# Kernel tuning notes

Hardware: AMD Instinct MI355X
Metric: run time of the kernel (lower is better)

The kernel has to match this reference:

```python
import jax, jax.numpy as jnp
import numpy as np

B, CIN, COUT, H, W, K, SDIM = 16, 256, 256, 64, 64, 3, 128

def setup_inputs() -> dict:
    key = jax.random.key(0)
    ks = jax.random.split(key, 5)
    return {
        "x": jax.random.normal(ks[0], (B, CIN, H, W), dtype=jnp.float32),
        "c_src": jax.random.normal(ks[1], (B, SDIM), dtype=jnp.float32),
        "c_trg": jax.random.normal(ks[2], (B, SDIM), dtype=jnp.float32),
        "style_w": jax.random.normal(ks[3], (CIN, SDIM), dtype=jnp.float32),
        "style_b": jnp.ones((CIN,), dtype=jnp.float32),  # bias_init=1
        "weight": jax.random.normal(ks[4], (1, COUT, CIN, K, K), dtype=jnp.float32),
    }

def reference(x, c_src, c_trg, style_w, style_b, weight):
    b, cin, h, w = x.shape
    _, cout, _, k, _ = weight.shape
    # EqualLinear: scale = 1/sqrt(dim_in)=1/sqrt(128), lr_mul=1
    lin_scale = np.float32(1.0 / np.sqrt(SDIM))
    s = c_trg @ (style_w * lin_scale).T + style_b            # [B, Cin]
    # modulate
    conv_scale = np.float32(1.0 / np.sqrt(cin * k * k))
    wmod = conv_scale * weight * s[:, None, :, None, None]   # [B, Cout, Cin, K, K]
    # demodulate
    demod = jax.lax.rsqrt(jnp.sum(wmod * wmod, axis=(2, 3, 4)) + 1e-8)  # [B, Cout]
    wmod = wmod * demod[:, :, None, None, None]
    # grouped conv with groups=batch == per-sample conv; vmap over batch
    def conv_one(xb, wb):
        # xb: [Cin,H,W], wb: [Cout,Cin,K,K]
        return jax.lax.conv_general_dilated(
            xb[None], wb, window_strides=(1, 1), padding="SAME",
            dimension_numbers=("NCHW", "OIHW", "NCHW"))[0]
    out = jax.vmap(conv_one)(x, wmod)                        # [B, Cout, H, W]
    return out
```

## Files before the change

kernel.cpp:

```cpp
#include <hip/hip_runtime.h>


#define WSH_OFF    35684352
#define S_OFF      36864000
#define G_OFF      36880384
#define DEMOD_OFF  37142528

typedef __attribute__((ext_vector_type(8))) short bf16x8;
typedef __attribute__((ext_vector_type(4))) float f32x4;
typedef __attribute__((ext_vector_type(4))) int i32x4;

#define GLOAD_LDS16(g, l)                                                        \
  __builtin_amdgcn_global_load_lds(                                              \
      (const __attribute__((address_space(1))) void*)(g),                        \
      (__attribute__((address_space(3))) void*)(l), 16, 0, 0)

__device__ __forceinline__ unsigned short f2bf(float f) {
  unsigned int u = __builtin_bit_cast(unsigned int, f);
  u += 0x7FFFu + ((u >> 16) & 1u);
  return (unsigned short)(u >> 16);
}

__global__ void prep1_k(const float* __restrict__ c_trg,
                        const float* __restrict__ style_w,
                        const float* __restrict__ style_b,
                        const float* __restrict__ weight,
                        float* __restrict__ s,
                        short* __restrict__ wsh,
                        float* __restrict__ G) {
  const int blk = blockIdx.x;
  const int tid = threadIdx.x;
  if (blk < 16) {
    const int b = blk;
    const float* ct = c_trg + b * 128;
    const float* sw = style_w + tid * 128;
    float acc = 0.f;
#pragma unroll 4
    for (int d = 0; d < 128; ++d) acc += ct[d] * sw[d];
    s[b * 256 + tid] = acc * 0.08838834764831845f + style_b[tid];
  } else {
    const int idx = (blk - 16) * 256 + tid;
    const float* wsrc = weight + idx * 9;
    float g = 0.f;
#pragma unroll
    for (int t = 0; t < 9; ++t) {
      float v = wsrc[t] * 0.020833333333333332f;
      g += v * v;
      wsh[t * 65536 + idx] = (short)f2bf(v);
    }
    G[idx] = g;
  }
}

__global__ void xpose_k(const float* __restrict__ x,
                        const float* __restrict__ s,
                        const float* __restrict__ G,
                        short* __restrict__ xpad,
                        float* __restrict__ demod) {
  __shared__ float tile[64][65];
  const int bid = blockIdx.x;
  const int tid = threadIdx.x;
  if (bid >= 4112) {
    const int id = bid - 4112;
    const int b = id >> 8, co = id & 255;
    const float sv = s[b * 256 + tid];
    float ss = G[co * 256 + tid] * sv * sv;
#pragma unroll
    for (int o = 32; o; o >>= 1) ss += __shfl_down(ss, o);
    __shared__ float red[4];
    if ((tid & 63) == 0) red[tid >> 6] = ss;
    __syncthreads();
    if (tid == 0) demod[id] = rsqrtf(red[0] + red[1] + red[2] + red[3] + 1e-8f);
    return;
  }
  if (bid >= 4096) {
    const int b = bid - 4096;
    char* base = (char*)xpad + b * 66 * 66 * 512;
    const i32x4 z = {0, 0, 0, 0};
    for (int i = tid; i < 4224; i += 256) {
      const int r = i >= 2112;
      const int off = r * (65 * 66 * 512) + (i - r * 2112) * 16;
      *(i32x4*)(base + off) = z;
    }
    for (int i = tid; i < 4096; i += 256) {
      const int h = 1 + (i >> 6);
      const int side = (i >> 5) & 1;
      const int j = i & 31;
      *(i32x4*)(base + (h * 66 + side * 65) * 512 + j * 16) = z;
    }
    return;
  }
  const int ct = bid & 3;
  const int h = (bid >> 2) & 63;
  const int b = bid >> 8;
  const int w = tid & 63, cl = tid >> 6;
  const float* src = x + ((b * 256 + ct * 64) * 64 + h) * 64;
#pragma unroll
  for (int i = 0; i < 16; ++i) {
    int c = i * 4 + cl;
    tile[c][w] = src[c * 4096 + w];
  }
  const int cp = tid & 31;
  const float s0 = s[b * 256 + ct * 64 + cp * 2];
  const float s1 = s[b * 256 + ct * 64 + cp * 2 + 1];
  __syncthreads();
  short* dst = xpad + ((b * 66 + h + 1) * 66 + 1) * 256 + ct * 64;
#pragma unroll
  for (int i = 0; i < 8; ++i) {
    int idx = i * 256 + tid;
    int w2 = idx >> 5;
    unsigned int u = (unsigned int)f2bf(tile[cp * 2][w2] * s0) |
                     ((unsigned int)f2bf(tile[cp * 2 + 1][w2] * s1) << 16);
    *(unsigned int*)(dst + w2 * 256 + cp * 2) = u;
  }
}

__global__ __launch_bounds__(512, 2) void conv_k(const short* __restrict__ xpad,
                                                 const short* __restrict__ wsh,
                                                 const float* __restrict__ demod,
                                                 float* __restrict__ out) {
  extern __shared__ __align__(16) char lds[];

  const int tid = threadIdx.x;
  const int lane = tid & 63;
  const int wid = tid >> 6;
  const int wm = wid >> 2;
  const int wn = wid & 3;

  const int orig = blockIdx.x;
  const int bid = (orig & 7) * 32 + (orig >> 3);
  const int b = bid >> 4;
  const int r0 = (bid & 15) * 4;

  const int t3 = tid >> 3;
  const int c16 = (tid & 7) * 16;
  const int swzc = c16 ^ ((t3 & 7) << 4);
  int aO[4], bO[4];
#pragma unroll
  for (int j = 0; j < 4; ++j) {
    aO[j] = (j * 64 + t3) * 512 + swzc;
    bO[j] = ((b * 66 + r0 + j) * 66 + t3) * 512 + swzc;
  }
  const char* wB = (const char*)wsh;
  const char* xB = (const char*)xpad;

  auto stageA = [&](int ts) {
    const int tap = ts >> 2, cc = ts & 3;
    const int aAdd = tap * 131072 + cc * 128;
    char* d = lds + (ts & 1) * 65536;
#pragma unroll
    for (int j = 0; j < 4; ++j)
      GLOAD_LDS16(wB + aAdd + aO[j], d + j * 8192 + tid * 16);
  };
  auto stageB = [&](int ts) {
    const int tap = ts >> 2, cc = ts & 3;
    const int dh = (tap * 11) >> 5;
    const int bAdd = (dh * 66 + (tap - dh * 3)) * 512 + cc * 128;
    char* d = lds + (ts & 1) * 65536 + 32768;
#pragma unroll
    for (int j = 0; j < 4; ++j)
      GLOAD_LDS16(xB + bAdd + bO[j], d + j * 8192 + tid * 16);
  };

  const int xall = (lane & 7) << 4;
  const int xl = xall & 0x30;
  const int xh = xall & 0x40;
  const int colR = (((lane >> 4) << 4) ^ xl);
  const int ko0 = xh;
  const int ko1 = 64 ^ xh;
  const int aRdBase = (wm * 128 + (lane & 15)) * 128 + colR;
  const int bRdBase = 32768 + (wn * 64 + (lane & 15)) * 128 + colR;

  f32x4 acc[8][4] = {};

  stageA(0);
  stageB(0);

  for (int t = 0; t < 36; ++t) {
    asm volatile("s_waitcnt vmcnt(0)" ::: "memory");
    __builtin_amdgcn_s_barrier();
    __builtin_amdgcn_sched_barrier(0);

    const char* Ab = lds + (t & 1) * 65536 + aRdBase;
    const char* Bb = lds + (t & 1) * 65536 + bRdBase;
    bf16x8 a03[4][2], a47[4][2], bq[4][2];

#pragma unroll
    for (int m = 0; m < 4; ++m) a03[m][0] = *(const bf16x8*)(Ab + m * 2048 + ko0);
#pragma unroll
    for (int n = 0; n < 4; ++n) bq[n][0] = *(const bf16x8*)(Bb + n * 2048 + ko0);
    if (t + 1 < 36) stageA(t + 1);
    __builtin_amdgcn_sched_barrier(0);

#pragma unroll
    for (int m = 0; m < 4; ++m) a03[m][1] = *(const bf16x8*)(Ab + m * 2048 + ko1);
#pragma unroll
    for (int n = 0; n < 4; ++n) bq[n][1] = *(const bf16x8*)(Bb + n * 2048 + ko1);
    if (t + 1 < 36) stageB(t + 1);
    __builtin_amdgcn_sched_barrier(0);

#pragma unroll
    for (int m = 0; m < 4; ++m)
#pragma unroll
      for (int n = 0; n < 4; ++n)
        acc[m][n] = __builtin_amdgcn_mfma_f32_16x16x32_bf16(a03[m][0], bq[n][0], acc[m][n], 0, 0, 0);
    __builtin_amdgcn_sched_barrier(0);

#pragma unroll
    for (int m = 0; m < 4; ++m) a47[m][0] = *(const bf16x8*)(Ab + (m + 4) * 2048 + ko0);
    __builtin_amdgcn_sched_barrier(0);

#pragma unroll
    for (int m = 0; m < 4; ++m)
#pragma unroll
      for (int n = 0; n < 4; ++n)
        acc[m][n] = __builtin_amdgcn_mfma_f32_16x16x32_bf16(a03[m][1], bq[n][1], acc[m][n], 0, 0, 0);
    __builtin_amdgcn_sched_barrier(0);

#pragma unroll
    for (int m = 0; m < 4; ++m) a47[m][1] = *(const bf16x8*)(Ab + (m + 4) * 2048 + ko1);
    __builtin_amdgcn_sched_barrier(0);

#pragma unroll
    for (int m = 0; m < 4; ++m)
#pragma unroll
      for (int n = 0; n < 4; ++n)
        acc[m + 4][n] = __builtin_amdgcn_mfma_f32_16x16x32_bf16(a47[m][0], bq[n][0], acc[m + 4][n], 0, 0, 0);
    __builtin_amdgcn_sched_barrier(0);

#pragma unroll
    for (int m = 0; m < 4; ++m)
#pragma unroll
      for (int n = 0; n < 4; ++n)
        acc[m + 4][n] = __builtin_amdgcn_mfma_f32_16x16x32_bf16(a47[m][1], bq[n][1], acc[m + 4][n], 0, 0, 0);
    asm volatile("" ::: "memory");
  }

  const int pc = lane & 15;
  const int rOff = (lane >> 4) * 4;
  const int h = r0 + wn;
#pragma unroll
  for (int m = 0; m < 8; ++m) {
#pragma unroll
    for (int r = 0; r < 4; ++r) {
      const int co = wm * 128 + m * 16 + rOff + r;
      const float dm = demod[(b << 8) + co];
      float* orow = out + (((b << 8) + co) << 12) + (h << 6);
#pragma unroll
      for (int n = 0; n < 4; ++n) {
        orow[n * 16 + pc] = acc[m][n][r] * dm;
      }
    }
  }
}

extern "C" void kernel_launch(void* const* d_in, const int* in_sizes, int n_in,
                              void* d_out, int out_size, void* d_ws, size_t ws_size,
                              hipStream_t stream) {
  const float* x       = (const float*)d_in[0];
  const float* c_trg   = (const float*)d_in[2];
  const float* style_w = (const float*)d_in[3];
  const float* style_b = (const float*)d_in[4];
  const float* weight  = (const float*)d_in[5];
  float* out = (float*)d_out;

  char* ws = (char*)d_ws;
  short* xpad  = (short*)(ws);
  short* wsh   = (short*)(ws + WSH_OFF);
  float* s     = (float*)(ws + S_OFF);
  float* G     = (float*)(ws + G_OFF);
  float* demod = (float*)(ws + DEMOD_OFF);

  hipFuncSetAttribute((const void*)conv_k,
                      hipFuncAttributeMaxDynamicSharedMemorySize, 131072);

  prep1_k<<<272, 256, 0, stream>>>(c_trg, style_w, style_b, weight, s, wsh, G);
  xpose_k<<<8208, 256, 0, stream>>>(x, s, G, xpad, demod);
  conv_k<<<256, 512, 131072, stream>>>(xpad, wsh, demod, out);
}
```

Before: 99.22 us.

## Load weight fragments directly from global memory instead of staging through LDS

The A operand (pre-transformed weights) is now read straight from global memory into registers for each tap and channel chunk, and the LDS double-buffering covers only the input tile. This halves LDS use and removes the LDS write/read traffic for weights, which could allow higher occupancy. It also drops the sched_barrier fences so the compiler can interleave loads and MFMAs freely. The risk is exposing global/L2 latency on the weight loads, since they are no longer prefetched one step ahead, plus less controlled instruction scheduling.

```diff
diff --git a/kernel.cpp b/kernel.cpp
--- a/kernel.cpp
+++ b/kernel.cpp
@@ -135,28 +135,18 @@
   const int t3 = tid >> 3;
   const int c16 = (tid & 7) * 16;
   const int swzc = c16 ^ ((t3 & 7) << 4);
-  int aO[4], bO[4];
-#pragma unroll
-  for (int j = 0; j < 4; ++j) {
-    aO[j] = (j * 64 + t3) * 512 + swzc;
+  int bO[4];
+#pragma unroll
+  for (int j = 0; j < 4; ++j)
     bO[j] = ((b * 66 + r0 + j) * 66 + t3) * 512 + swzc;
-  }
   const char* wB = (const char*)wsh;
   const char* xB = (const char*)xpad;
 
-  auto stageA = [&](int ts) {
-    const int tap = ts >> 2, cc = ts & 3;
-    const int aAdd = tap * 131072 + cc * 128;
-    char* d = lds + (ts & 1) * 65536;
-#pragma unroll
-    for (int j = 0; j < 4; ++j)
-      GLOAD_LDS16(wB + aAdd + aO[j], d + j * 8192 + tid * 16);
-  };
   auto stageB = [&](int ts) {
     const int tap = ts >> 2, cc = ts & 3;
     const int dh = (tap * 11) >> 5;
     const int bAdd = (dh * 66 + (tap - dh * 3)) * 512 + cc * 128;
-    char* d = lds + (ts & 1) * 65536 + 32768;
+    char* d = lds + (ts & 1) * 32768;
 #pragma unroll
     for (int j = 0; j < 4; ++j)
       GLOAD_LDS16(xB + bAdd + bO[j], d + j * 8192 + tid * 16);
@@ -168,12 +158,12 @@
   const int colR = (((lane >> 4) << 4) ^ xl);
   const int ko0 = xh;
   const int ko1 = 64 ^ xh;
-  const int aRdBase = (wm * 128 + (lane & 15)) * 128 + colR;
-  const int bRdBase = 32768 + (wn * 64 + (lane & 15)) * 128 + colR;
+  const int bRdBase = (wn * 64 + (lane & 15)) * 128 + colR;
+
+  const int aBase = (wm * 128 + (lane & 15)) * 512 + (lane >> 4) * 16;
 
   f32x4 acc[8][4] = {};
 
-  stageA(0);
   stageB(0);
 
   for (int t = 0; t < 36; ++t) {
@@ -181,58 +171,53 @@
     __builtin_amdgcn_s_barrier();
     __builtin_amdgcn_sched_barrier(0);
 
-    const char* Ab = lds + (t & 1) * 65536 + aRdBase;
-    const char* Bb = lds + (t & 1) * 65536 + bRdBase;
+    const int tap = t >> 2, cc = t & 3;
+    const char* aT = wB + tap * 131072 + cc * 128 + aBase;
+    const char* Bb = lds + (t & 1) * 32768 + bRdBase;
     bf16x8 a03[4][2], a47[4][2], bq[4][2];
 
 #pragma unroll
-    for (int m = 0; m < 4; ++m) a03[m][0] = *(const bf16x8*)(Ab + m * 2048 + ko0);
-#pragma unroll
-    for (int n = 0; n < 4; ++n) bq[n][0] = *(const bf16x8*)(Bb + n * 2048 + ko0);
-    if (t + 1 < 36) stageA(t + 1);
-    __builtin_amdgcn_sched_barrier(0);
-
-#pragma unroll
-    for (int m = 0; m < 4; ++m) a03[m][1] = *(const bf16x8*)(Ab + m * 2048 + ko1);
-#pragma unroll
-    for (int n = 0; n < 4; ++n) bq[n][1] = *(const bf16x8*)(Bb + n * 2048 + ko1);
+    for (int m = 0; m < 4; ++m) {
+      a03[m][0] = *(const bf16x8*)(aT + m * 8192);
+      a03[m][1] = *(const bf16x8*)(aT + m * 8192 + 64);
+    }
+#pragma unroll
+    for (int n = 0; n < 4; ++n) {
+      bq[n][0] = *(const bf16x8*)(Bb + n * 2048 + ko0);
+      bq[n][1] = *(const bf16x8*)(Bb + n * 2048 + ko1);
+    }
     if (t + 1 < 36) stageB(t + 1);
-    __builtin_amdgcn_sched_barrier(0);
 
 #pragma unroll
     for (int m = 0; m < 4; ++m)
 #pragma unroll
       for (int n = 0; n < 4; ++n)
         acc[m][n] = __builtin_amdgcn_mfma_f32_16x16x32_bf16(a03[m][0], bq[n][0], acc[m][n], 0, 0, 0);
-    __builtin_amdgcn_sched_barrier(0);
-
-#pragma unroll
-    for (int m = 0; m < 4; ++m) a47[m][0] = *(const bf16x8*)(Ab + (m + 4) * 2048 + ko0);
-    __builtin_amdgcn_sched_barrier(0);
+
+#pragma unroll
+    for (int m = 0; m < 4; ++m) {
+      a47[m][0] = *(const bf16x8*)(aT + (m + 4) * 8192);
+      a47[m][1] = *(const bf16x8*)(aT + (m + 4) * 8192 + 64);
+    }
 
 #pragma unroll
     for (int m = 0; m < 4; ++m)
 #pragma unroll
       for (int n = 0; n < 4; ++n)
         acc[m][n] = __builtin_amdgcn_mfma_f32_16x16x32_bf16(a03[m][1], bq[n][1], acc[m][n], 0, 0, 0);
-    __builtin_amdgcn_sched_barrier(0);
-
-#pragma unroll
-    for (int m = 0; m < 4; ++m) a47[m][1] = *(const bf16x8*)(Ab + (m + 4) * 2048 + ko1);
-    __builtin_amdgcn_sched_barrier(0);
 
 #pragma unroll
     for (int m = 0; m < 4; ++m)
 #pragma unroll
       for (int n = 0; n < 4; ++n)
         acc[m + 4][n] = __builtin_amdgcn_mfma_f32_16x16x32_bf16(a47[m][0], bq[n][0], acc[m + 4][n], 0, 0, 0);
-    __builtin_amdgcn_sched_barrier(0);
 
 #pragma unroll
     for (int m = 0; m < 4; ++m)
 #pragma unroll
       for (int n = 0; n < 4; ++n)
         acc[m + 4][n] = __builtin_amdgcn_mfma_f32_16x16x32_bf16(a47[m][1], bq[n][1], acc[m + 4][n], 0, 0, 0);
+
     asm volatile("" ::: "memory");
   }
 
@@ -272,9 +257,9 @@
   float* demod = (float*)(ws + DEMOD_OFF);
 
   hipFuncSetAttribute((const void*)conv_k,
-                      hipFuncAttributeMaxDynamicSharedMemorySize, 131072);
+                      hipFuncAttributeMaxDynamicSharedMemorySize, 65536);
 
   prep1_k<<<272, 256, 0, stream>>>(c_trg, style_w, style_b, weight, s, wsh, G);
   xpose_k<<<8208, 256, 0, stream>>>(x, s, G, xpad, demod);
-  conv_k<<<256, 512, 131072, stream>>>(xpad, wsh, demod, out);
-}
+  conv_k<<<256, 512, 65536, stream>>>(xpad, wsh, demod, out);
+}
```

Result: slower. 190.5 us (+92.0%).

## Halve conv workgroup to 4 waves with 128x128 per-wave tiles

Applied to the files above, without the earlier changes.

The conv kernel moves from 8 waves of 512 threads, each computing a 128x64 tile, to 4 waves of 256 threads, each computing a 128x128 tile with 256 accumulator registers. Staging loads double per thread to cover the same LDS tile. The interleaved sched_barrier schedule is replaced by two plain load-then-MFMA phases per K step. Each wave now reuses fragments over more MFMAs, at the cost of fewer waves to hide latency and heavy register pressure that could spill.

```diff
diff --git a/kernel.cpp b/kernel.cpp
--- a/kernel.cpp
+++ b/kernel.cpp
@@ -115,7 +115,7 @@
   }
 }
 
-__global__ __launch_bounds__(512, 2) void conv_k(const short* __restrict__ xpad,
+__global__ __launch_bounds__(256, 1) void conv_k(const short* __restrict__ xpad,
                                                  const short* __restrict__ wsh,
                                                  const float* __restrict__ demod,
                                                  float* __restrict__ out) {
@@ -124,8 +124,8 @@
   const int tid = threadIdx.x;
   const int lane = tid & 63;
   const int wid = tid >> 6;
-  const int wm = wid >> 2;
-  const int wn = wid & 3;
+  const int wm = wid >> 1;
+  const int wn = wid & 1;
 
   const int orig = blockIdx.x;
   const int bid = (orig & 7) * 32 + (orig >> 3);
@@ -135,11 +135,12 @@
   const int t3 = tid >> 3;
   const int c16 = (tid & 7) * 16;
   const int swzc = c16 ^ ((t3 & 7) << 4);
-  int aO[4], bO[4];
-#pragma unroll
-  for (int j = 0; j < 4; ++j) {
-    aO[j] = (j * 64 + t3) * 512 + swzc;
-    bO[j] = ((b * 66 + r0 + j) * 66 + t3) * 512 + swzc;
+  int aO[8], bO[8];
+#pragma unroll
+  for (int j = 0; j < 8; ++j) {
+    const int p = j * 32 + t3;
+    aO[j] = p * 512 + swzc;
+    bO[j] = ((b * 66 + r0 + (p >> 6)) * 66 + (p & 63)) * 512 + swzc;
   }
   const char* wB = (const char*)wsh;
   const char* xB = (const char*)xpad;
@@ -149,8 +150,8 @@
     const int aAdd = tap * 131072 + cc * 128;
     char* d = lds + (ts & 1) * 65536;
 #pragma unroll
-    for (int j = 0; j < 4; ++j)
-      GLOAD_LDS16(wB + aAdd + aO[j], d + j * 8192 + tid * 16);
+    for (int j = 0; j < 8; ++j)
+      GLOAD_LDS16(wB + aAdd + aO[j], d + j * 4096 + tid * 16);
   };
   auto stageB = [&](int ts) {
     const int tap = ts >> 2, cc = ts & 3;
@@ -158,8 +159,8 @@
     const int bAdd = (dh * 66 + (tap - dh * 3)) * 512 + cc * 128;
     char* d = lds + (ts & 1) * 65536 + 32768;
 #pragma unroll
-    for (int j = 0; j < 4; ++j)
-      GLOAD_LDS16(xB + bAdd + bO[j], d + j * 8192 + tid * 16);
+    for (int j = 0; j < 8; ++j)
+      GLOAD_LDS16(xB + bAdd + bO[j], d + j * 4096 + tid * 16);
   };
 
   const int xall = (lane & 7) << 4;
@@ -169,9 +170,9 @@
   const int ko0 = xh;
   const int ko1 = 64 ^ xh;
   const int aRdBase = (wm * 128 + (lane & 15)) * 128 + colR;
-  const int bRdBase = 32768 + (wn * 64 + (lane & 15)) * 128 + colR;
-
-  f32x4 acc[8][4] = {};
+  const int bRdBase = 32768 + (wn * 128 + (lane & 15)) * 128 + colR;
+
+  f32x4 acc[8][8] = {};
 
   stageA(0);
   stageB(0);
@@ -183,72 +184,47 @@
 
     const char* Ab = lds + (t & 1) * 65536 + aRdBase;
     const char* Bb = lds + (t & 1) * 65536 + bRdBase;
-    bf16x8 a03[4][2], a47[4][2], bq[4][2];
-
-#pragma unroll
-    for (int m = 0; m < 4; ++m) a03[m][0] = *(const bf16x8*)(Ab + m * 2048 + ko0);
-#pragma unroll
-    for (int n = 0; n < 4; ++n) bq[n][0] = *(const bf16x8*)(Bb + n * 2048 + ko0);
+    bf16x8 af[8], bq[8];
+
+#pragma unroll
+    for (int m = 0; m < 8; ++m) af[m] = *(const bf16x8*)(Ab + m * 2048 + ko0);
+#pragma unroll
+    for (int n = 0; n < 8; ++n) bq[n] = *(const bf16x8*)(Bb + n * 2048 + ko0);
     if (t + 1 < 36) stageA(t + 1);
-    __builtin_amdgcn_sched_barrier(0);
-
-#pragma unroll
-    for (int m = 0; m < 4; ++m) a03[m][1] = *(const bf16x8*)(Ab + m * 2048 + ko1);
-#pragma unroll
-    for (int n = 0; n < 4; ++n) bq[n][1] = *(const bf16x8*)(Bb + n * 2048 + ko1);
+#pragma unroll
+    for (int m = 0; m < 8; ++m)
+#pragma unroll
+      for (int n = 0; n < 8; ++n)
+        acc[m][n] = __builtin_amdgcn_mfma_f32_16x16x32_bf16(af[m], bq[n], acc[m][n], 0, 0, 0);
+
+#pragma unroll
+    for (int m = 0; m < 8; ++m) af[m] = *(const bf16x8*)(Ab + m * 2048 + ko1);
+#pragma unroll
+    for (int n = 0; n < 8; ++n) bq[n] = *(const bf16x8*)(Bb + n * 2048 + ko1);
     if (t + 1 < 36) stageB(t + 1);
-    __builtin_amdgcn_sched_barrier(0);
-
-#pragma unroll
-    for (int m = 0; m < 4; ++m)
-#pragma unroll
-      for (int n = 0; n < 4; ++n)
-        acc[m][n] = __builtin_amdgcn_mfma_f32_16x16x32_bf16(a03[m][0], bq[n][0], acc[m][n], 0, 0, 0);
-    __builtin_amdgcn_sched_barrier(0);
-
-#pragma unroll
-    for (int m = 0; m < 4; ++m) a47[m][0] = *(const bf16x8*)(Ab + (m + 4) * 2048 + ko0);
-    __builtin_amdgcn_sched_barrier(0);
-
-#pragma unroll
-    for (int m = 0; m < 4; ++m)
-#pragma unroll
-      for (int n = 0; n < 4; ++n)
-        acc[m][n] = __builtin_amdgcn_mfma_f32_16x16x32_bf16(a03[m][1], bq[n][1], acc[m][n], 0, 0, 0);
-    __builtin_amdgcn_sched_barrier(0);
-
-#pragma unroll
-    for (int m = 0; m < 4; ++m) a47[m][1] = *(const bf16x8*)(Ab + (m + 4) * 2048 + ko1);
-    __builtin_amdgcn_sched_barrier(0);
-
-#pragma unroll
-    for (int m = 0; m < 4; ++m)
-#pragma unroll
-      for (int n = 0; n < 4; ++n)
-        acc[m + 4][n] = __builtin_amdgcn_mfma_f32_16x16x32_bf16(a47[m][0], bq[n][0], acc[m + 4][n], 0, 0, 0);
-    __builtin_amdgcn_sched_barrier(0);
-
-#pragma unroll
-    for (int m = 0; m < 4; ++m)
-#pragma unroll
-      for (int n = 0; n < 4; ++n)
-        acc[m + 4][n] = __builtin_amdgcn_mfma_f32_16x16x32_bf16(a47[m][1], bq[n][1], acc[m + 4][n], 0, 0, 0);
+#pragma unroll
+    for (int m = 0; m < 8; ++m)
+#pragma unroll
+      for (int n = 0; n < 8; ++n)
+        acc[m][n] = __builtin_amdgcn_mfma_f32_16x16x32_bf16(af[m], bq[n], acc[m][n], 0, 0, 0);
+
     asm volatile("" ::: "memory");
   }
 
   const int pc = lane & 15;
   const int rOff = (lane >> 4) * 4;
-  const int h = r0 + wn;
 #pragma unroll
   for (int m = 0; m < 8; ++m) {
 #pragma unroll
     for (int r = 0; r < 4; ++r) {
       const int co = wm * 128 + m * 16 + rOff + r;
       const float dm = demod[(b << 8) + co];
-      float* orow = out + (((b << 8) + co) << 12) + (h << 6);
-#pragma unroll
-      for (int n = 0; n < 4; ++n) {
-        orow[n * 16 + pc] = acc[m][n][r] * dm;
+      float* obase = out + (((b << 8) + co) << 12);
+#pragma unroll
+      for (int n = 0; n < 8; ++n) {
+        const int pix = wn * 128 + n * 16 + pc;
+        const int h = r0 + (pix >> 6), w = pix & 63;
+        obase[(h << 6) + w] = acc[m][n][r] * dm;
       }
     }
   }
@@ -276,5 +252,5 @@
 
   prep1_k<<<272, 256, 0, stream>>>(c_trg, style_w, style_b, weight, s, wsh, G);
   xpose_k<<<8208, 256, 0, stream>>>(x, s, G, xpad, demod);
-  conv_k<<<256, 512, 131072, stream>>>(xpad, wsh, demod, out);
-}
+  conv_k<<<256, 256, 131072, stream>>>(xpad, wsh, demod, out);
+}
```

Result: slower. 177.1 us (+78.5%).

## Software-pipeline second K-half MFMAs across iterations with register double buffering

Applied to the files above, without the earlier changes.

Restructures the main loop so the MFMAs for the second K-half of each tile are deferred into the next iteration, where they overlap the LDS reads for that iteration's first half. An extra barrier is placed after the first-half reads, and both global-to-LDS stage loads are issued together after the second-half reads. A tail block after the loop finishes the final deferred MFMAs. The aim is better overlap of LDS reads with matrix math. In exchange it holds more bf16 fragments live in registers and adds a second barrier per iteration, which may reduce occupancy.

```diff
diff --git a/kernel.cpp b/kernel.cpp
--- a/kernel.cpp
+++ b/kernel.cpp
@@ -172,6 +172,7 @@
   const int bRdBase = 32768 + (wn * 64 + (lane & 15)) * 128 + colR;
 
   f32x4 acc[8][4] = {};
+  bf16x8 a1[8], b1[4];
 
   stageA(0);
   stageB(0);
@@ -183,58 +184,45 @@
 
     const char* Ab = lds + (t & 1) * 65536 + aRdBase;
     const char* Bb = lds + (t & 1) * 65536 + bRdBase;
-    bf16x8 a03[4][2], a47[4][2], bq[4][2];
-
-#pragma unroll
-    for (int m = 0; m < 4; ++m) a03[m][0] = *(const bf16x8*)(Ab + m * 2048 + ko0);
-#pragma unroll
-    for (int n = 0; n < 4; ++n) bq[n][0] = *(const bf16x8*)(Bb + n * 2048 + ko0);
-    if (t + 1 < 36) stageA(t + 1);
+    bf16x8 a0[8], b0[4];
+
+#pragma unroll
+    for (int m = 0; m < 8; ++m) a0[m] = *(const bf16x8*)(Ab + m * 2048 + ko0);
+#pragma unroll
+    for (int n = 0; n < 4; ++n) b0[n] = *(const bf16x8*)(Bb + n * 2048 + ko0);
+    if (t > 0) {
+#pragma unroll
+      for (int m = 0; m < 8; ++m)
+#pragma unroll
+        for (int n = 0; n < 4; ++n)
+          acc[m][n] = __builtin_amdgcn_mfma_f32_16x16x32_bf16(a1[m], b1[n], acc[m][n], 0, 0, 0);
+    }
+
+    __builtin_amdgcn_s_barrier();
     __builtin_amdgcn_sched_barrier(0);
 
 #pragma unroll
-    for (int m = 0; m < 4; ++m) a03[m][1] = *(const bf16x8*)(Ab + m * 2048 + ko1);
-#pragma unroll
-    for (int n = 0; n < 4; ++n) bq[n][1] = *(const bf16x8*)(Bb + n * 2048 + ko1);
-    if (t + 1 < 36) stageB(t + 1);
-    __builtin_amdgcn_sched_barrier(0);
-
-#pragma unroll
-    for (int m = 0; m < 4; ++m)
+    for (int m = 0; m < 8; ++m) a1[m] = *(const bf16x8*)(Ab + m * 2048 + ko1);
+#pragma unroll
+    for (int n = 0; n < 4; ++n) b1[n] = *(const bf16x8*)(Bb + n * 2048 + ko1);
+    if (t + 1 < 36) {
+      stageA(t + 1);
+      stageB(t + 1);
+    }
+#pragma unroll
+    for (int m = 0; m < 8; ++m)
 #pragma unroll
       for (int n = 0; n < 4; ++n)
-        acc[m][n] = __builtin_amdgcn_mfma_f32_16x16x32_bf16(a03[m][0], bq[n][0], acc[m][n], 0, 0, 0);
-    __builtin_amdgcn_sched_barrier(0);
-
-#pragma unroll
-    for (int m = 0; m < 4; ++m) a47[m][0] = *(const bf16x8*)(Ab + (m + 4) * 2048 + ko0);
-    __builtin_amdgcn_sched_barrier(0);
-
-#pragma unroll
-    for (int m = 0; m < 4; ++m)
-#pragma unroll
-      for (int n = 0; n < 4; ++n)
-        acc[m][n] = __builtin_amdgcn_mfma_f32_16x16x32_bf16(a03[m][1], bq[n][1], acc[m][n], 0, 0, 0);
-    __builtin_amdgcn_sched_barrier(0);
-
-#pragma unroll
-    for (int m = 0; m < 4; ++m) a47[m][1] = *(const bf16x8*)(Ab + (m + 4) * 2048 + ko1);
-    __builtin_amdgcn_sched_barrier(0);
-
-#pragma unroll
-    for (int m = 0; m < 4; ++m)
-#pragma unroll
-      for (int n = 0; n < 4; ++n)
-        acc[m + 4][n] = __builtin_amdgcn_mfma_f32_16x16x32_bf16(a47[m][0], bq[n][0], acc[m + 4][n], 0, 0, 0);
-    __builtin_amdgcn_sched_barrier(0);
-
-#pragma unroll
-    for (int m = 0; m < 4; ++m)
-#pragma unroll
-      for (int n = 0; n < 4; ++n)
-        acc[m + 4][n] = __builtin_amdgcn_mfma_f32_16x16x32_bf16(a47[m][1], bq[n][1], acc[m + 4][n], 0, 0, 0);
+        acc[m][n] = __builtin_amdgcn_mfma_f32_16x16x32_bf16(a0[m], b0[n], acc[m][n], 0, 0, 0);
+
     asm volatile("" ::: "memory");
   }
+
+#pragma unroll
+  for (int m = 0; m < 8; ++m)
+#pragma unroll
+    for (int n = 0; n < 4; ++n)
+      acc[m][n] = __builtin_amdgcn_mfma_f32_16x16x32_bf16(a1[m], b1[n], acc[m][n], 0, 0, 0);
 
   const int pc = lane & 15;
   const int rOff = (lane >> 4) * 4;
```

Measured after the change: 102.7 us. 3.5% more time.
